# Optimization experiments

Hardware: AMD Instinct MI355X
Metric: run time of the kernel (lower is better)

Reference implementation:

```python
import jax, jax.numpy as jnp
import numpy as np

B, LQ, LK, D = 32, 1024, 1024, 256

def setup_inputs() -> dict:
    key = jax.random.key(0)
    ks = jax.random.split(key, 7)
    return {
        "raw_query": jax.random.normal(ks[0], (B, LQ, D), dtype=jnp.float32),
        "raw_key": jax.random.normal(ks[1], (B, LK, D), dtype=jnp.float32),
        "raw_value": jax.random.normal(ks[2], (B, LK, D), dtype=jnp.float32),
        "value_mask": jax.random.randint(ks[3], (B, LQ), 0, 2, dtype=jnp.int32),
        "WQ": jax.random.normal(ks[4], (D, D), dtype=jnp.float32) * 0.05,
        "WK": jax.random.normal(ks[5], (D, D), dtype=jnp.float32) * 0.05,
        "WV": jax.random.normal(ks[6], (D, D), dtype=jnp.float32) * 0.05,
    }

def reference(raw_query, raw_key, raw_value, value_mask, WQ, WK, WV):
    # Projections: [B, L, D] @ [D, D]
    Q = raw_query @ WQ
    K = raw_key @ WK
    V = raw_value @ WV
    # Scores: [B, LQ, LK] (use_scale=False -> no 1/sqrt(d_k))
    att = jnp.einsum("bqd,bkd->bqk", Q, K)
    # Mask expanded on axis=2 -> zeroes entire query rows of scores (faithful to tf.where+zeros_like)
    att = jnp.where(value_mask[:, :, None] > 0, att, jnp.zeros((), dtype=att.dtype))
    att = jax.nn.softmax(att, axis=-1)
    # Output: [B, LQ, D]
    return jnp.einsum("bqk,bkd->bqd", att, V)
```

## Files before the change

kernel.cpp:

```cpp
#include <hip/hip_runtime.h>
#include <hip/hip_bf16.h>
#include <math.h>

#define B_ 32
#define L_ 1024
#define D_ 256

typedef _Float16 half8 __attribute__((ext_vector_type(8)));
typedef __fp16   fp16x2 __attribute__((ext_vector_type(2)));
typedef short    s16x8 __attribute__((ext_vector_type(8)));
typedef float    f32x4 __attribute__((ext_vector_type(4)));

typedef __attribute__((address_space(3))) unsigned int lds_u32;
typedef __attribute__((address_space(1))) unsigned int gbl_u32;

__device__ __forceinline__ void gl_lds16(const void* g, void* l) {
    __builtin_amdgcn_global_load_lds((gbl_u32*)g, (lds_u32*)l, 16, 0, 0);
}

__device__ __forceinline__ unsigned short f2bf(float x) {
    unsigned u = __float_as_uint(x);
    u += 0x7FFFu + ((u >> 16) & 1u);
    return (unsigned short)(u >> 16);
}

__device__ __forceinline__ unsigned short f2h(float x) {
    _Float16 h = (_Float16)x;
    unsigned short u;
    __builtin_memcpy(&u, &h, 2);
    return u;
}

__device__ __forceinline__ unsigned pkrtz(float a, float b) {
    fp16x2 v = __builtin_amdgcn_cvt_pkrtz(a, b);
    unsigned u;
    __builtin_memcpy(&u, &v, 4);
    return u;
}

__global__ __launch_bounds__(256) void wprep_kernel(
    const float* __restrict__ W0, const float* __restrict__ W1,
    const float* __restrict__ W2, unsigned short* __restrict__ Wt)
{
    const int z = blockIdx.z;
    const float* __restrict__ W = (z == 0) ? W0 : (z == 1) ? W1 : W2;
    __shared__ unsigned short T[64][72];
    const int k0 = blockIdx.x << 6, n0 = blockIdx.y << 6;
    const int t = threadIdx.x;
    const int r = t >> 2, c0 = (t & 3) << 4;
    #pragma unroll
    for (int j = 0; j < 16; j += 4) {
        float4 w4 = *(const float4*)(W + (size_t)(k0 + r) * 256 + n0 + c0 + j);
        T[c0 + j + 0][r] = f2h(w4.x);
        T[c0 + j + 1][r] = f2h(w4.y);
        T[c0 + j + 2][r] = f2h(w4.z);
        T[c0 + j + 3][r] = f2h(w4.w);
    }
    __syncthreads();
    const int n = t >> 2, kc = (t & 3) << 4;
    unsigned short* dst = Wt + ((size_t)z << 16) + (size_t)(n0 + n) * 256 + k0 + kc;
    *(uint4*)(dst + 0) = *(const uint4*)&T[n][kc + 0];
    *(uint4*)(dst + 8) = *(const uint4*)&T[n][kc + 8];
}

__global__ __launch_bounds__(512, 4) void proj_mfma_kernel(
    const float* __restrict__ A0, const float* __restrict__ A1,
    const float* __restrict__ A2, const unsigned short* __restrict__ Wt,
    unsigned short* __restrict__ Qh, unsigned short* __restrict__ Kh,
    unsigned short* __restrict__ Vt)
{
    __shared__ unsigned short SMEM[32768];
    unsigned short* Asm = SMEM;
    unsigned short* Bsm = SMEM + 16384;

    const int fblk = blockIdx.x;
    const int xcd = fblk & 7;
    const int g   = fblk >> 3;
    const int y   = g & 1;
    const int p   = g >> 1;
    const int z   = p >> 5;
    const int xl  = p & 31;
    const int xt  = (xcd << 5) + xl;
    const int bm = xt << 7, bn = y << 7;

    const float* __restrict__ A = (z == 0) ? A0 : (z == 1) ? A1 : A2;
    const int t = threadIdx.x, lane = t & 63, w = t >> 6;
    const int wm = (w >> 1) << 5, wn = (w & 1) << 6;

    const float* __restrict__ Ag = A + (size_t)bm * 256;
    const unsigned short* __restrict__ Bg = Wt + ((size_t)z << 16) + (size_t)bn * 256;

    f32x4 acc[2][4];
    const f32x4 z4 = {0.f, 0.f, 0.f, 0.f};
    #pragma unroll
    for (int mi = 0; mi < 2; ++mi)
        #pragma unroll
        for (int ni = 0; ni < 4; ++ni) acc[mi][ni] = z4;

    const int ar = t >> 2, ac4 = t & 3;
    float4 aA[4], aB[4];

#define LOADA(itv, AR)                                                          \
    {                                                                           \
        _Pragma("unroll")                                                       \
        for (int i = 0; i < 4; ++i)                                             \
            AR[i] = *(const float4*)(Ag + (size_t)ar * 256 + ((itv) << 6)       \
                                     + (ac4 << 4) + (i << 2));                  \
    }
#define WRITEA(buf, AR)                                                         \
    {                                                                           \
        _Pragma("unroll")                                                       \
        for (int i = 0; i < 2; ++i) {                                           \
            int c  = (ac4 << 1) + i;                                            \
            int cs = c ^ (ar & 7);                                              \
            uint4 d;                                                            \
            d.x = pkrtz(AR[2 * i].x,     AR[2 * i].y);                          \
            d.y = pkrtz(AR[2 * i].z,     AR[2 * i].w);                          \
            d.z = pkrtz(AR[2 * i + 1].x, AR[2 * i + 1].y);                      \
            d.w = pkrtz(AR[2 * i + 1].z, AR[2 * i + 1].w);                      \
            *(uint4*)&Asm[((buf) << 13) + (ar << 6) + (cs << 3)] = d;           \
        }                                                                       \
    }

    auto stageB = [&](int buf, int it) {
        #pragma unroll
        for (int i = 0; i < 2; ++i) {
            int o = (i << 9) + t;
            int r = o >> 3, c = o & 7;
            int cs = c ^ (r & 7);
            gl_lds16(Bg + (size_t)r * 256 + (it << 6) + (cs << 3),
                     &Bsm[(buf << 13) + (o << 3)]);
        }
    };
    auto compute = [&](int buf) {
        #pragma unroll
        for (int kc = 0; kc < 2; ++kc) {
            half8 af[2], bfr[4];
            #pragma unroll
            for (int mi = 0; mi < 2; ++mi) {
                int m = wm + (mi << 4) + (lane & 15);
                int cs = ((kc << 2) + (lane >> 4)) ^ (m & 7);
                af[mi] = *(const half8*)&Asm[(buf << 13) + (m << 6) + (cs << 3)];
            }
            #pragma unroll
            for (int ni = 0; ni < 4; ++ni) {
                int n = wn + (ni << 4) + (lane & 15);
                int cs = ((kc << 2) + (lane >> 4)) ^ (n & 7);
                bfr[ni] = *(const half8*)&Bsm[(buf << 13) + (n << 6) + (cs << 3)];
            }
            #pragma unroll
            for (int mi = 0; mi < 2; ++mi)
                #pragma unroll
                for (int ni = 0; ni < 4; ++ni)
                    acc[mi][ni] = __builtin_amdgcn_mfma_f32_16x16x32_f16(
                        af[mi], bfr[ni], acc[mi][ni], 0, 0, 0);
        }
    };

    LOADA(0, aA);
    WRITEA(0, aA);
    stageB(0, 0);
    LOADA(1, aB);
    __syncthreads();

    LOADA(2, aA);
    WRITEA(1, aB);
    stageB(1, 1);
    compute(0);
    __syncthreads();
    LOADA(3, aB);
    WRITEA(0, aA);
    stageB(0, 2);
    compute(1);
    __syncthreads();
    WRITEA(1, aB);
    stageB(1, 3);
    compute(0);
    __syncthreads();
    compute(1);

#undef LOADA
#undef WRITEA

    if (z < 2) {
        unsigned short* __restrict__ C = (z == 0) ? Qh : Kh;
        __syncthreads();
        unsigned short (*Cs)[136] = (unsigned short(*)[136])SMEM;
        #pragma unroll
        for (int mi = 0; mi < 2; ++mi) {
            int q0l = wm + (mi << 4) + ((lane >> 4) << 2);
            #pragma unroll
            for (int ni = 0; ni < 4; ++ni) {
                int cl = wn + (ni << 4) + (lane & 15);
                #pragma unroll
                for (int r = 0; r < 4; ++r)
                    Cs[q0l + r][cl] = f2h(acc[mi][ni][r]);
            }
        }
        __syncthreads();
        #pragma unroll
        for (int i = 0; i < 4; ++i) {
            int o = (i << 9) + t;
            int r = o >> 4, c = o & 15;
            *(uint4*)(C + (size_t)(bm + r) * 256 + bn + (c << 3)) =
                *(const uint4*)&Cs[r][c << 3];
        }
    } else {
        __syncthreads();
        unsigned short (*Tt)[144] = (unsigned short(*)[144])SMEM;
        #pragma unroll
        for (int mi = 0; mi < 2; ++mi) {
            int m0 = wm + (mi << 4) + ((lane >> 4) << 2);
            #pragma unroll
            for (int ni = 0; ni < 4; ++ni) {
                int n = wn + (ni << 4) + (lane & 15);
                #pragma unroll
                for (int r = 0; r < 4; ++r)
                    Tt[n][m0 + r] = f2bf(acc[mi][ni][r]);
            }
        }
        __syncthreads();
        const int bb = bm >> 10, kin = bm & 1023;
        const int dr = t >> 2, cb = (t & 3) << 5;
        unsigned short* dst = Vt + ((size_t)bb * 256 + bn + dr) * 1024 + kin + cb;
        #pragma unroll
        for (int j = 0; j < 4; ++j)
            *(uint4*)(dst + (j << 3)) = *(const uint4*)&Tt[dr][cb + (j << 3)];
    }
}

__global__ __launch_bounds__(1024, 4) void fused_attn_kernel(
    const unsigned short* __restrict__ Qh, const unsigned short* __restrict__ Kh,
    const unsigned short* __restrict__ Vt, const int* __restrict__ mask,
    float* __restrict__ Out)
{
    __shared__ unsigned short Ks[2][16384];
    __shared__ unsigned short Vs[2][16384];
    __shared__ unsigned short Ps[128 * 64];
    float* lredp = (float*)Ps;

    const int f  = blockIdx.x;
    const int b  = (f & 7) + ((f >> 6) << 3);
    const int q0 = ((f >> 3) & 7) << 7;
    const size_t bL = (size_t)b * L_;
    const int t = threadIdx.x, lane = t & 63, w = t >> 6;
    const int wm_s = (w >> 1) << 4, wn_s = (w & 1) << 5;
    const int wm_v = (w >> 2) << 5, wn_v = (w & 3) << 6;

    const unsigned short* __restrict__ Kb = Kh + (bL << 8);
    const unsigned short* __restrict__ Vb = Vt + (bL << 8);

    auto stageK = [&](int buf, int kt) {
        #pragma unroll
        for (int i = 0; i < 2; ++i) {
            int o = (i << 10) + t;
            int r = o >> 5, c = o & 31;
            int cs = (c & 24) | ((c & 7) ^ (r & 7));
            gl_lds16(Kb + (size_t)((kt << 6) + r) * 256 + (cs << 3), &Ks[buf][o << 3]);
        }
    };
    auto stageV = [&](int buf, int kt) {
        #pragma unroll
        for (int i = 0; i < 2; ++i) {
            int o = (i << 10) + t;
            int d = o >> 3, c = o & 7;
            int cs = c ^ (d & 7);
            gl_lds16(Vb + ((size_t)d << 10) + (kt << 6) + (cs << 3), &Vs[buf][o << 3]);
        }
    };

    stageK(0, 0);
    stageV(0, 0);

    half8 qf[8];
    {
        int m = wm_s + (lane & 15);
        const unsigned short* qp = Qh + ((bL + q0 + m) << 8) + ((lane >> 4) << 3);
        #pragma unroll
        for (int kc = 0; kc < 8; ++kc)
            qf[kc] = *(const half8*)(qp + (kc << 5));
    }
    int mv[4];
    {
        int qrow = wm_s + ((lane >> 4) << 2);
        #pragma unroll
        for (int r = 0; r < 4; ++r) mv[r] = mask[bL + q0 + qrow + r];
    }

    f32x4 o_acc[2][4];
    const f32x4 z4 = {0.f, 0.f, 0.f, 0.f};
    #pragma unroll
    for (int mi = 0; mi < 2; ++mi)
        #pragma unroll
        for (int ni = 0; ni < 4; ++ni) o_acc[mi][ni] = z4;
    float lacc[4] = {};

    __syncthreads();

    for (int kt = 0; kt < 16; ++kt) {
        const int cur = kt & 1;
        if (kt < 15) stageV(cur ^ 1, kt + 1);

        f32x4 accs[2];
        accs[0] = z4; accs[1] = z4;
        #pragma unroll
        for (int kc = 0; kc < 8; ++kc) {
            int kb = (kc >> 1) << 6, cc = ((kc & 1) << 2) + (lane >> 4);
            int n0 = wn_s + (lane & 15);
            int n1 = n0 + 16;
            half8 bf0 = *(const half8*)&Ks[cur][(n0 << 8) + kb + ((cc ^ (n0 & 7)) << 3)];
            half8 bf1 = *(const half8*)&Ks[cur][(n1 << 8) + kb + ((cc ^ (n1 & 7)) << 3)];
            accs[0] = __builtin_amdgcn_mfma_f32_16x16x32_f16(qf[kc], bf0, accs[0], 0, 0, 0);
            accs[1] = __builtin_amdgcn_mfma_f32_16x16x32_f16(qf[kc], bf1, accs[1], 0, 0, 0);
        }

        {
            int qrow = wm_s + ((lane >> 4) << 2);
            #pragma unroll
            for (int ni = 0; ni < 2; ++ni) {
                int kl = wn_s + (ni << 4) + (lane & 15);
                #pragma unroll
                for (int r = 0; r < 4; ++r) {
                    int q = qrow + r;
                    float p = mv[r] ? __expf(accs[ni][r]) : 1.0f;
                    Ps[(q << 6) + ((((kl >> 3) ^ (q & 7)) << 3)) + (kl & 7)] = f2bf(p);
                    lacc[r] += p;
                }
            }
        }
        __syncthreads();

        if (kt < 15) stageK(cur ^ 1, kt + 1);

        #pragma unroll
        for (int kc2 = 0; kc2 < 2; ++kc2) {
            s16x8 pa[2], vb[4];
            int cc = (kc2 << 2) + (lane >> 4);
            #pragma unroll
            for (int mi = 0; mi < 2; ++mi) {
                int m = wm_v + (mi << 4) + (lane & 15);
                pa[mi] = *(const s16x8*)&Ps[(m << 6) + ((cc ^ (m & 7)) << 3)];
            }
            #pragma unroll
            for (int ni = 0; ni < 4; ++ni) {
                int n = wn_v + (ni << 4) + (lane & 15);
                vb[ni] = *(const s16x8*)&Vs[cur][(n << 6) + ((cc ^ (n & 7)) << 3)];
            }
            #pragma unroll
            for (int mi = 0; mi < 2; ++mi)
                #pragma unroll
                for (int ni = 0; ni < 4; ++ni)
                    o_acc[mi][ni] = __builtin_amdgcn_mfma_f32_16x16x32_bf16(
                        pa[mi], vb[ni], o_acc[mi][ni], 0, 0, 0);
        }
        __syncthreads();
    }

    #pragma unroll
    for (int r = 0; r < 4; ++r) {
        float v = lacc[r];
        v += __shfl_xor(v, 1);
        v += __shfl_xor(v, 2);
        v += __shfl_xor(v, 4);
        v += __shfl_xor(v, 8);
        if ((lane & 15) == 0)
            lredp[((wm_s + ((lane >> 4) << 2) + r) << 1) + (w & 1)] = v;
    }
    __syncthreads();

    #pragma unroll
    for (int mi = 0; mi < 2; ++mi) {
        #pragma unroll
        for (int rr = 0; rr < 4; ++rr) {
            int q = wm_v + (mi << 4) + ((lane >> 4) << 2) + rr;
            float inv = 1.0f / (lredp[q << 1] + lredp[(q << 1) + 1]);
            #pragma unroll
            for (int ni = 0; ni < 4; ++ni) {
                int d = wn_v + (ni << 4) + (lane & 15);
                Out[((bL + q0 + q) << 8) + d] = o_acc[mi][ni][rr] * inv;
            }
        }
    }
}

extern "C" void kernel_launch(void* const* d_in, const int* in_sizes, int n_in,
                              void* d_out, int out_size, void* d_ws, size_t ws_size,
                              hipStream_t stream) {
    const float* rq = (const float*)d_in[0];
    const float* rk = (const float*)d_in[1];
    const float* rv = (const float*)d_in[2];
    const int*   vm = (const int*)d_in[3];
    const float* WQ = (const float*)d_in[4];
    const float* WK = (const float*)d_in[5];
    const float* WV = (const float*)d_in[6];
    float* out = (float*)d_out;

    char* ws = (char*)d_ws;
    unsigned short* Qh = (unsigned short*)(ws);
    unsigned short* Kh = (unsigned short*)(ws + ((size_t)16 << 20));
    unsigned short* Vt = (unsigned short*)(ws + ((size_t)32 << 20));
    unsigned short* Wt = (unsigned short*)(ws + ((size_t)48 << 20));

    dim3 wg(4, 4, 3);
    wprep_kernel<<<wg, 256, 0, stream>>>(WQ, WK, WV, Wt);

    proj_mfma_kernel<<<1536, 512, 0, stream>>>(rq, rk, rv, Wt, Qh, Kh, Vt);

    fused_attn_kernel<<<256, 1024, 0, stream>>>(Qh, Kh, Vt, vm, out);
}
```

Baseline: 89.89 us.

## Widen projection tiles to full 256 output columns with 1024-thread blocks

The projection GEMM now has each block compute a 128x256 output tile covering all output columns, instead of two blocks each computing 128x128. The block grows to 1024 threads (16 waves), which halves the grid. Each fp32 activation row is therefore read and converted to fp16 once instead of twice, removing redundant global A traffic. In exchange the kernel needs more LDS and a two-pass transpose epilogue for V, drops the XCD-aware block remapping, and fewer, larger blocks may lower occupancy.

Result: no change. 90.42 us (+0.6%).

```diff
diff --git a/kernel.cpp b/kernel.cpp
--- a/kernel.cpp
+++ b/kernel.cpp
@@ -63,32 +63,27 @@
     *(uint4*)(dst + 8) = *(const uint4*)&T[n][kc + 8];
 }
 
-__global__ __launch_bounds__(512, 4) void proj_mfma_kernel(
+__global__ __launch_bounds__(1024, 4) void proj_mfma_kernel(
     const float* __restrict__ A0, const float* __restrict__ A1,
     const float* __restrict__ A2, const unsigned short* __restrict__ Wt,
     unsigned short* __restrict__ Qh, unsigned short* __restrict__ Kh,
     unsigned short* __restrict__ Vt)
 {
-    __shared__ unsigned short SMEM[32768];
+    __shared__ unsigned short SMEM[49152];
     unsigned short* Asm = SMEM;
     unsigned short* Bsm = SMEM + 16384;
 
     const int fblk = blockIdx.x;
-    const int xcd = fblk & 7;
-    const int g   = fblk >> 3;
-    const int y   = g & 1;
-    const int p   = g >> 1;
-    const int z   = p >> 5;
-    const int xl  = p & 31;
-    const int xt  = (xcd << 5) + xl;
-    const int bm = xt << 7, bn = y << 7;
+    const int xt = fblk & 255;
+    const int z  = fblk >> 8;
+    const int bm = xt << 7;
 
     const float* __restrict__ A = (z == 0) ? A0 : (z == 1) ? A1 : A2;
     const int t = threadIdx.x, lane = t & 63, w = t >> 6;
-    const int wm = (w >> 1) << 5, wn = (w & 1) << 6;
+    const int wm = (w >> 2) << 5, wn = (w & 3) << 6;
 
     const float* __restrict__ Ag = A + (size_t)bm * 256;
-    const unsigned short* __restrict__ Bg = Wt + ((size_t)z << 16) + (size_t)bn * 256;
+    const unsigned short* __restrict__ Bg = Wt + ((size_t)z << 16);
 
     f32x4 acc[2][4];
     const f32x4 z4 = {0.f, 0.f, 0.f, 0.f};
@@ -97,39 +92,34 @@
         #pragma unroll
         for (int ni = 0; ni < 4; ++ni) acc[mi][ni] = z4;
 
-    const int ar = t >> 2, ac4 = t & 3;
-    float4 aA[4], aB[4];
+    const int ar = t >> 3, ac = t & 7;
+    float4 aA[2], aB[2];
 
 #define LOADA(itv, AR)                                                          \
     {                                                                           \
-        _Pragma("unroll")                                                       \
-        for (int i = 0; i < 4; ++i)                                             \
-            AR[i] = *(const float4*)(Ag + (size_t)ar * 256 + ((itv) << 6)       \
-                                     + (ac4 << 4) + (i << 2));                  \
+        const float* ap = Ag + (size_t)ar * 256 + ((itv) << 6) + (ac << 3);     \
+        AR[0] = *(const float4*)ap;                                             \
+        AR[1] = *(const float4*)(ap + 4);                                       \
     }
 #define WRITEA(buf, AR)                                                         \
     {                                                                           \
-        _Pragma("unroll")                                                       \
-        for (int i = 0; i < 2; ++i) {                                           \
-            int c  = (ac4 << 1) + i;                                            \
-            int cs = c ^ (ar & 7);                                              \
-            uint4 d;                                                            \
-            d.x = pkrtz(AR[2 * i].x,     AR[2 * i].y);                          \
-            d.y = pkrtz(AR[2 * i].z,     AR[2 * i].w);                          \
-            d.z = pkrtz(AR[2 * i + 1].x, AR[2 * i + 1].y);                      \
-            d.w = pkrtz(AR[2 * i + 1].z, AR[2 * i + 1].w);                      \
-            *(uint4*)&Asm[((buf) << 13) + (ar << 6) + (cs << 3)] = d;           \
-        }                                                                       \
+        uint4 d;                                                                \
+        d.x = pkrtz(AR[0].x, AR[0].y);                                          \
+        d.y = pkrtz(AR[0].z, AR[0].w);                                          \
+        d.z = pkrtz(AR[1].x, AR[1].y);                                          \
+        d.w = pkrtz(AR[1].z, AR[1].w);                                          \
+        int cs = ac ^ (ar & 7);                                                 \
+        *(uint4*)&Asm[((buf) << 13) + (ar << 6) + (cs << 3)] = d;               \
     }
 
     auto stageB = [&](int buf, int it) {
         #pragma unroll
         for (int i = 0; i < 2; ++i) {
-            int o = (i << 9) + t;
+            int o = (i << 10) + t;
             int r = o >> 3, c = o & 7;
             int cs = c ^ (r & 7);
             gl_lds16(Bg + (size_t)r * 256 + (it << 6) + (cs << 3),
-                     &Bsm[(buf << 13) + (o << 3)]);
+                     &Bsm[(buf << 14) + (o << 3)]);
         }
     };
     auto compute = [&](int buf) {
@@ -146,7 +136,7 @@
             for (int ni = 0; ni < 4; ++ni) {
                 int n = wn + (ni << 4) + (lane & 15);
                 int cs = ((kc << 2) + (lane >> 4)) ^ (n & 7);
-                bfr[ni] = *(const half8*)&Bsm[(buf << 13) + (n << 6) + (cs << 3)];
+                bfr[ni] = *(const half8*)&Bsm[(buf << 14) + (n << 6) + (cs << 3)];
             }
             #pragma unroll
             for (int mi = 0; mi < 2; ++mi)
@@ -185,7 +175,7 @@
     if (z < 2) {
         unsigned short* __restrict__ C = (z == 0) ? Qh : Kh;
         __syncthreads();
-        unsigned short (*Cs)[136] = (unsigned short(*)[136])SMEM;
+        unsigned short (*Cs)[264] = (unsigned short(*)[264])SMEM;
         #pragma unroll
         for (int mi = 0; mi < 2; ++mi) {
             int q0l = wm + (mi << 4) + ((lane >> 4) << 2);
@@ -200,32 +190,37 @@
         __syncthreads();
         #pragma unroll
         for (int i = 0; i < 4; ++i) {
-            int o = (i << 9) + t;
-            int r = o >> 4, c = o & 15;
-            *(uint4*)(C + (size_t)(bm + r) * 256 + bn + (c << 3)) =
+            int o = (i << 10) + t;
+            int r = o >> 5, c = o & 31;
+            *(uint4*)(C + (size_t)(bm + r) * 256 + (c << 3)) =
                 *(const uint4*)&Cs[r][c << 3];
         }
     } else {
-        __syncthreads();
-        unsigned short (*Tt)[144] = (unsigned short(*)[144])SMEM;
-        #pragma unroll
-        for (int mi = 0; mi < 2; ++mi) {
-            int m0 = wm + (mi << 4) + ((lane >> 4) << 2);
-            #pragma unroll
-            for (int ni = 0; ni < 4; ++ni) {
-                int n = wn + (ni << 4) + (lane & 15);
+        unsigned short (*Tt)[136] = (unsigned short(*)[136])SMEM;
+        const int bb = bm >> 10, kin = bm & 1023;
+        #pragma unroll
+        for (int dh = 0; dh < 2; ++dh) {
+            __syncthreads();
+            if (((w & 3) >> 1) == dh) {
                 #pragma unroll
-                for (int r = 0; r < 4; ++r)
-                    Tt[n][m0 + r] = f2bf(acc[mi][ni][r]);
-            }
-        }
-        __syncthreads();
-        const int bb = bm >> 10, kin = bm & 1023;
-        const int dr = t >> 2, cb = (t & 3) << 5;
-        unsigned short* dst = Vt + ((size_t)bb * 256 + bn + dr) * 1024 + kin + cb;
-        #pragma unroll
-        for (int j = 0; j < 4; ++j)
-            *(uint4*)(dst + (j << 3)) = *(const uint4*)&Tt[dr][cb + (j << 3)];
+                for (int mi = 0; mi < 2; ++mi) {
+                    int m0 = wm + (mi << 4) + ((lane >> 4) << 2);
+                    #pragma unroll
+                    for (int ni = 0; ni < 4; ++ni) {
+                        int nl = (wn & 127) + (ni << 4) + (lane & 15);
+                        #pragma unroll
+                        for (int r = 0; r < 4; ++r)
+                            Tt[nl][m0 + r] = f2bf(acc[mi][ni][r]);
+                    }
+                }
+            }
+            __syncthreads();
+            int dr = t >> 3, cq = t & 7;
+            unsigned short* dst = Vt + ((size_t)bb * 256 + (dh << 7) + dr) * 1024
+                                  + kin + (cq << 4);
+            *(uint4*)(dst + 0) = *(const uint4*)&Tt[dr][(cq << 4) + 0];
+            *(uint4*)(dst + 8) = *(const uint4*)&Tt[dr][(cq << 4) + 8];
+        }
     }
 }
 
@@ -404,7 +399,7 @@
     dim3 wg(4, 4, 3);
     wprep_kernel<<<wg, 256, 0, stream>>>(WQ, WK, WV, Wt);
 
-    proj_mfma_kernel<<<1536, 512, 0, stream>>>(rq, rk, rv, Wt, Qh, Kh, Vt);
+    proj_mfma_kernel<<<768, 1024, 0, stream>>>(rq, rk, rv, Wt, Qh, Kh, Vt);
 
     fused_attn_kernel<<<256, 1024, 0, stream>>>(Qh, Kh, Vt, vm, out);
 }
```
